# Kernel optimization log

Measured on AMD Instinct MI355X. Metric: run time of the kernel, lower is better.

The kernel has to match this reference:

```python
import jax, jax.numpy as jnp
import numpy as np

EMBED_DIM = 768
N_HEADS = 12
HEAD_DIM = EMBED_DIM // N_HEADS
SCALE = HEAD_DIM ** 0.5


def setup_inputs() -> dict:
    key = jax.random.key(0)
    k1, k2, k3 = jax.random.split(key, 3)
    x = jax.random.normal(k1, (2, 2048, EMBED_DIM), dtype=jnp.float32)
    # weights stored [in, out] so forward is x @ W (equivalent to torch Linear with W.T)
    w_qkv = jax.random.normal(k2, (EMBED_DIM, 3 * EMBED_DIM), dtype=jnp.float32) * (EMBED_DIM ** -0.5)
    w_proj = jax.random.normal(k3, (EMBED_DIM, EMBED_DIM), dtype=jnp.float32) * (EMBED_DIM ** -0.5)
    return {"x": x, "w_qkv": w_qkv, "w_proj": w_proj}


def reference(x, w_qkv, w_proj):
    B, N, C = x.shape
    qkv = x @ w_qkv  # [B, N, 3C]
    qkv = qkv.reshape(B, N, 3, N_HEADS, HEAD_DIM)
    qkv = jnp.transpose(qkv, (2, 0, 3, 1, 4))  # [3, B, H, N, hd]
    q, k, v = qkv[0], qkv[1], qkv[2]
    attn = jnp.einsum("bhnd,bhmd->bhnm", q, k) / SCALE  # [B, H, N, N]
    attn = jax.nn.softmax(attn, axis=-1)
    out = jnp.einsum("bhnm,bhmd->bhnd", attn, v)  # [B, H, N, hd]
    out = jnp.transpose(out, (0, 2, 1, 3)).reshape(B, N, C)
    return out @ w_proj
```

## Files before the change

kernel.cpp:

```cpp
#include <hip/hip_runtime.h>
#include <hip/hip_bf16.h>
#include <stdint.h>

typedef uint16_t u16;
typedef __attribute__((ext_vector_type(4))) float f32x4;
typedef __attribute__((ext_vector_type(8))) short bf16x8;

#define LOG2E 1.4426950408889634f

static __device__ __forceinline__ u16 f2b(float x){
  union { float f; uint32_t u; } a; a.f = x;
  uint32_t r = a.u + 0x7FFFu + ((a.u >> 16) & 1u);
  return (u16)(r >> 16);
}

static __device__ __forceinline__ uint32_t pkrhu(float lo, float hi){
  union { float f; uint32_t u; } a, b; a.f = lo; b.f = hi;
  return __builtin_amdgcn_perm(b.u + 0x8000u, a.u + 0x8000u, 0x07060302u);
}

#define GLD16(g, l) __builtin_amdgcn_global_load_lds((const __attribute__((address_space(1))) void*)(g), (__attribute__((address_space(3))) void*)(l), 16, 0, 0)

__global__ __launch_bounds__(256) void k_prep(const float* __restrict__ x, u16* __restrict__ Xb,
                                              const float* __restrict__ wqkv, u16* __restrict__ WqkvT,
                                              const float* __restrict__ wproj, u16* __restrict__ WprojT){
  __shared__ float t[32][33];
  const int bid = blockIdx.x, tid = threadIdx.x;
  if (bid < 1536){
    int i = bid * 256 + tid;
    const f32x4* p = (const f32x4*)(x + (size_t)i * 8);
    f32x4 a = p[0], b = p[1];
    u16 h[8];
#pragma unroll
    for (int j = 0; j < 4; ++j){ h[j] = f2b(a[j]); h[4+j] = f2b(b[j]); }
    *(bf16x8*)(Xb + (size_t)i * 8) = *(const bf16x8*)h;
    return;
  }
  const float* in; u16* out; int R, C, bx, by;
  if (bid < 1536 + 1728){
    int q = bid - 1536; in = wqkv; out = WqkvT; R = 768; C = 2304; bx = q % 72; by = q / 72;
  } else {
    int q = bid - 1536 - 1728; in = wproj; out = WprojT; R = 768; C = 768; bx = q % 24; by = q / 24;
  }
  int c0 = bx * 32, r0 = by * 32;
  int tx = tid & 31, ty = tid >> 5;
#pragma unroll
  for (int i = 0; i < 32; i += 8) t[ty + i][tx] = in[(size_t)(r0 + ty + i) * C + c0 + tx];
  __syncthreads();
#pragma unroll
  for (int i = 0; i < 32; i += 8) out[(size_t)(c0 + ty + i) * R + r0 + tx] = f2b(t[tx][ty + i]);
}

__global__ __launch_bounds__(256) void k_gemmqkv(const u16* __restrict__ A, const u16* __restrict__ Bt,
                                                 u16* __restrict__ Qp, u16* __restrict__ Kp, u16* __restrict__ Vtp){
  __shared__ __align__(16) u16 SM[14336];
  const int tid = threadIdx.x;
  const int w = tid >> 6, l = tid & 63;
  const int m0 = blockIdx.x * 128, n0 = blockIdx.y * 96;
  const int wm = (w >> 1) * 64, wn = (w & 1) * 48;
  const int lg = l >> 4, lr = l & 15;
  f32x4 acc[4][3] = {};

  const int tr = tid >> 2;
  const int soct = ((tid & 3) ^ (tr & 3)) * 8;
  const u16* a0 = A  + (size_t)(m0 + tr) * 768 + soct;
  const u16* a1 = A  + (size_t)(m0 + 64 + tr) * 768 + soct;
  const u16* b0 = Bt + (size_t)(n0 + tr) * 768 + soct;
  const u16* b1 = Bt + (size_t)(n0 + 64 + tr) * 768 + soct;
  u16* const A0d = SM + 0     + tid*8;  u16* const A0e = SM + 2048  + tid*8;
  u16* const A1d = SM + 4096  + tid*8;  u16* const A1e = SM + 6144  + tid*8;
  u16* const B0d = SM + 8192  + tid*8;  u16* const B0e = SM + 10240 + tid*8;
  u16* const B1d = SM + 11264 + tid*8;  u16* const B1e = SM + 13312 + tid*8;

#define QSTAGE0 do { GLD16(a0, A0d); GLD16(a1, A0e); GLD16(b0, B0d); if (tid < 128) GLD16(b1, B0e); \
                     a0 += 32; a1 += 32; b0 += 32; b1 += 32; } while(0)
#define QSTAGE1 do { GLD16(a0, A1d); GLD16(a1, A1e); GLD16(b0, B1d); if (tid < 128) GLD16(b1, B1e); \
                     a0 += 32; a1 += 32; b0 += 32; b1 += 32; } while(0)

  const int foct = (lg ^ (lr & 3)) * 8;

#define QCOMP(ABASE, BBASE) do {                                                            \
    bf16x8 af[4], bfr[3];                                                                   \
    _Pragma("unroll")                                                                       \
    for (int mf = 0; mf < 4; ++mf)                                                          \
      af[mf] = *(const bf16x8*)&SM[(ABASE) + (wm + mf*16 + lr) * 32 + foct];                \
    _Pragma("unroll")                                                                       \
    for (int nf = 0; nf < 3; ++nf)                                                          \
      bfr[nf] = *(const bf16x8*)&SM[(BBASE) + (wn + nf*16 + lr) * 32 + foct];               \
    _Pragma("unroll")                                                                       \
    for (int mf = 0; mf < 4; ++mf)                                                          \
      _Pragma("unroll")                                                                     \
      for (int nf = 0; nf < 3; ++nf)                                                        \
        acc[mf][nf] = __builtin_amdgcn_mfma_f32_16x16x32_bf16(af[mf], bfr[nf], acc[mf][nf], 0, 0, 0); \
  } while(0)

  QSTAGE0;
  __syncthreads();
  for (int i = 0; i < 12; ++i){
    QSTAGE1;
    QCOMP(0, 8192);
    __syncthreads();
    if (i < 11) QSTAGE0;
    QCOMP(4096, 11264);
    __syncthreads();
  }
#undef QSTAGE0
#undef QSTAGE1
#undef QCOMP

  const int which = n0 / 768;
  const int nl0 = n0 - which * 768;
  if (which < 2){
    u16* dst = (which == 0) ? Qp : Kp;
    const float sc = (which == 0) ? 0.125f * LOG2E : 1.0f;
#pragma unroll
    for (int mf = 0; mf < 4; ++mf)
#pragma unroll
      for (int nf = 0; nf < 3; ++nf)
#pragma unroll
        for (int r = 0; r < 4; ++r){
          int m = m0 + wm + mf*16 + lg*4 + r;
          int n = nl0 + wn + nf*16 + lr;
          int b = m >> 11, row = m & 2047, hh = n >> 6, d = n & 63;
          dst[(size_t)((b*12 + hh)*2048 + row) * 64 + d] = f2b(acc[mf][nf][r] * sc);
        }
  } else {
#pragma unroll
    for (int mf = 0; mf < 4; ++mf)
#pragma unroll
      for (int nf = 0; nf < 3; ++nf)
#pragma unroll
        for (int r = 0; r < 4; ++r){
          int mrow = wm + mf*16 + lg*4 + r;
          int c    = wn + nf*16 + lr;
          SM[c * 128 + mrow] = f2b(acc[mf][nf][r]);
        }
    __syncthreads();
#pragma unroll
    for (int rr = 0; rr < 6; ++rr){
      int c  = rr*16 + (tid >> 4);
      int mo = (tid & 15) * 8;
      bf16x8 v = *(const bf16x8*)&SM[c * 128 + mo];
      int n = nl0 + c, hh = n >> 6, d = n & 63;
      int m = m0 + mo, b = m >> 11, key = m & 2047;
      *(bf16x8*)&Vtp[(size_t)((b*12 + hh)*64 + d) * 2048 + key] = v;
    }
  }
}

__global__ __launch_bounds__(256) void k_gemm64(const u16* __restrict__ A, const u16* __restrict__ Bt,
                                                float* __restrict__ Co){
  __shared__ __align__(16) u16 SM[8192];
  u16* Al = SM; u16* Bl = SM + 4096;
  const int tid = threadIdx.x;
  const int w = tid >> 6, l = tid & 63;
  const int m0 = blockIdx.x * 64, n0 = blockIdx.y * 64;
  const int wm = (w >> 1) * 32, wn = (w & 1) * 32;
  const int lg = l >> 4, lr = l & 15;
  f32x4 acc[2][2] = {};
  const u16* asrc = A  + (size_t)(m0 + w*16 + (l >> 3)) * 768 + (l & 7) * 8;
  const u16* bsrc = Bt + (size_t)(n0 + w*16 + (l >> 3)) * 768 + (l & 7) * 8;
  for (int k0 = 0; k0 < 768; k0 += 64){
#pragma unroll
    for (int i = 0; i < 2; ++i){
      GLD16(asrc + (size_t)(i*8)*768 + k0, &Al[(w*16 + i*8) * 64]);
      GLD16(bsrc + (size_t)(i*8)*768 + k0, &Bl[(w*16 + i*8) * 64]);
    }
    __syncthreads();
    bf16x8 af[2][2], bfr[2][2];
#pragma unroll
    for (int mf = 0; mf < 2; ++mf)
#pragma unroll
      for (int ks = 0; ks < 2; ++ks){
        af[mf][ks]  = *(const bf16x8*)&Al[(wm + mf*16 + lr) * 64 + ks*32 + lg*8];
        bfr[mf][ks] = *(const bf16x8*)&Bl[(wn + mf*16 + lr) * 64 + ks*32 + lg*8];
      }
#pragma unroll
    for (int ks = 0; ks < 2; ++ks)
#pragma unroll
      for (int mf = 0; mf < 2; ++mf)
#pragma unroll
        for (int nf = 0; nf < 2; ++nf)
          acc[mf][nf] = __builtin_amdgcn_mfma_f32_16x16x32_bf16(af[mf][ks], bfr[nf][ks], acc[mf][nf], 0, 0, 0);
    __syncthreads();
  }
#pragma unroll
  for (int mf = 0; mf < 2; ++mf)
#pragma unroll
    for (int nf = 0; nf < 2; ++nf)
#pragma unroll
      for (int r = 0; r < 4; ++r)
        Co[(size_t)(m0 + wm + mf*16 + lg*4 + r) * 768 + n0 + wn + nf*16 + lr] = acc[mf][nf][r];
}

__global__ __launch_bounds__(512, 3) void k_attn(const u16* __restrict__ Qp, const u16* __restrict__ Kp,
                                                 const u16* __restrict__ Vtp, u16* __restrict__ AO){
  __shared__ __align__(16) u16 SM[24576];
  const int tid = threadIdx.x, w = tid >> 6, l = tid & 63;
  const int QH = w >> 1, KH = w & 1;
  const int lg = l >> 4, lr = l & 15;
  const int qt_b = blockIdx.x, bh = blockIdx.y;
  const int b = bh / 12, hh = bh - b * 12;
  const size_t base = (size_t)bh * (2048 * 64);
  const u16* Qg = Qp + base; const u16* Kg = Kp + base; const u16* Vg = Vtp + base;
  const int q0w = qt_b * 64 + QH * 16;
  const int rsw = (lr & 7) * 8;

  bf16x8 qf[2];
#pragma unroll
  for (int ks = 0; ks < 2; ++ks)
    qf[ks] = *(const bf16x8*)&Qg[(size_t)(q0w + lr) * 64 + ks*32 + lg*8];

  f32x4 oacc[4] = {};
  float lp = 0.f;

  const int p_  = tid >> 3;
  const int sk  = 32*(p_ >> 5) + 8*((p_ >> 2) & 3) + 4*((p_ >> 4) & 1) + (p_ & 3);
  const int cs8 = (((tid & 7) ^ (p_ & 7)) << 3);
  const u16* kp = Kg + (size_t)sk * 64 + cs8;
  const u16* vp = Vg + ((size_t)p_ << 11) + cs8;
  const int drow = p_ * 64;
  u16* const K0 = SM + 0     + drow;  u16* const V0 = SM + 12288 + drow;
  u16* const K1 = SM + 4096  + drow;  u16* const V1 = SM + 16384 + drow;
  u16* const K2 = SM + 8192  + drow;  u16* const V2 = SM + 20480 + drow;

  auto compute = [&](const u16* Kc, const u16* Vc){
    f32x4 s[2] = {};
    bf16x8 kfr[2][2];
#pragma unroll
    for (int kf = 0; kf < 2; ++kf)
#pragma unroll
      for (int ks = 0; ks < 2; ++ks)
        kfr[kf][ks] = *(const bf16x8*)&Kc[(KH*32 + kf*16 + lr) * 64 + ((ks*32 + lg*8) ^ rsw)];
    __builtin_amdgcn_s_setprio(1);
#pragma unroll
    for (int ks = 0; ks < 2; ++ks)
#pragma unroll
      for (int kf = 0; kf < 2; ++kf)
        s[kf] = __builtin_amdgcn_mfma_f32_16x16x32_bf16(kfr[kf][ks], qf[ks], s[kf], 0, 0, 0);
    __builtin_amdgcn_s_setprio(0);

    float p00 = __builtin_exp2f(s[0][0]);
    float p01 = __builtin_exp2f(s[0][1]);
    float p02 = __builtin_exp2f(s[0][2]);
    float p03 = __builtin_exp2f(s[0][3]);
    float p10 = __builtin_exp2f(s[1][0]);
    float p11 = __builtin_exp2f(s[1][1]);
    float p12 = __builtin_exp2f(s[1][2]);
    float p13 = __builtin_exp2f(s[1][3]);
    lp += ((p00 + p01) + (p02 + p03)) + ((p10 + p11) + (p12 + p13));
    union { uint32_t u[4]; bf16x8 v; } fr;
    fr.u[0] = pkrhu(p00, p01);
    fr.u[1] = pkrhu(p02, p03);
    fr.u[2] = pkrhu(p10, p11);
    fr.u[3] = pkrhu(p12, p13);

    bf16x8 vfr[4];
#pragma unroll
    for (int nf = 0; nf < 4; ++nf)
      vfr[nf] = *(const bf16x8*)&Vc[(nf*16 + lr) * 64 + ((KH*32 + lg*8) ^ rsw)];
    __builtin_amdgcn_s_setprio(1);
#pragma unroll
    for (int nf = 0; nf < 4; ++nf)
      oacc[nf] = __builtin_amdgcn_mfma_f32_16x16x32_bf16(vfr[nf], fr.v, oacc[nf], 0, 0, 0);
    __builtin_amdgcn_s_setprio(0);
  };

#define STAGE2(KD, VD) do { GLD16(kp, KD); GLD16(vp, VD); kp += 4096; vp += 64; } while(0)
#define BAR_CNT2  do { asm volatile("s_waitcnt vmcnt(2)" ::: "memory"); \
                       __builtin_amdgcn_s_barrier(); __builtin_amdgcn_sched_barrier(0); } while(0)
#define BAR_CNT0  do { asm volatile("s_waitcnt vmcnt(0)" ::: "memory"); \
                       __builtin_amdgcn_s_barrier(); __builtin_amdgcn_sched_barrier(0); } while(0)

  STAGE2(K0, V0);
  STAGE2(K1, V1);
  BAR_CNT2;

  for (int g = 0; g < 10; ++g){
    STAGE2(K2, V2);  compute(SM + 0,    SM + 12288);  BAR_CNT2;
    STAGE2(K0, V0);  compute(SM + 4096, SM + 16384);  BAR_CNT2;
    STAGE2(K1, V1);  compute(SM + 8192, SM + 20480);  BAR_CNT2;
  }
  compute(SM + 0,    SM + 12288);
  BAR_CNT0;
  compute(SM + 4096, SM + 16384);

#undef STAGE2
#undef BAR_CNT2
#undef BAR_CNT0

  float lt = lp;
  lt += __shfl_xor(lt, 16);
  lt += __shfl_xor(lt, 32);

  __syncthreads();
  float* Osc = (float*)SM;
  float* Lsc = Osc + 64 * 65;
  if (KH == 1){
#pragma unroll
    for (int nf = 0; nf < 4; ++nf)
#pragma unroll
      for (int r = 0; r < 4; ++r)
        Osc[(QH*16 + lr) * 65 + nf*16 + lg*4 + r] = oacc[nf][r];
    if (lg == 0) Lsc[QH*16 + lr] = lt;
  }
  __syncthreads();
  if (KH == 0){
    float inv = 1.0f / (lt + Lsc[QH*16 + lr]);
#pragma unroll
    for (int nf = 0; nf < 4; ++nf)
#pragma unroll
      for (int r = 0; r < 4; ++r){
        float o = oacc[nf][r] + Osc[(QH*16 + lr) * 65 + nf*16 + lg*4 + r];
        AO[(size_t)((b << 11) + q0w + lr) * 768 + hh*64 + nf*16 + lg*4 + r] = f2b(o * inv);
      }
  }
}

extern "C" void kernel_launch(void* const* d_in, const int* in_sizes, int n_in,
                              void* d_out, int out_size, void* d_ws, size_t ws_size,
                              hipStream_t stream){
  const float* x      = (const float*)d_in[0];
  const float* w_qkv  = (const float*)d_in[1];
  const float* w_proj = (const float*)d_in[2];
  float* out = (float*)d_out;
  char* ws = (char*)d_ws;
  u16* Xb     = (u16*)(ws + 0);
  u16* WqkvT  = (u16*)(ws + 6291456);
  u16* WprojT = (u16*)(ws + 9830400);
  u16* Qp     = (u16*)(ws + 11010048);
  u16* Kp     = (u16*)(ws + 17301504);
  u16* Vtp    = (u16*)(ws + 23592960);
  u16* AO     = (u16*)(ws + 29884416);

  k_prep<<<3840, 256, 0, stream>>>(x, Xb, w_qkv, WqkvT, w_proj, WprojT);
  k_gemmqkv<<<dim3(32, 24), 256, 0, stream>>>(Xb, WqkvT, Qp, Kp, Vtp);
  k_attn<<<dim3(32, 24), 512, 0, stream>>>(Qp, Kp, Vtp, AO);
  k_gemm64<<<dim3(64, 12), 256, 0, stream>>>(AO, WprojT, out);
}
```

Before: 87.34 us.

## Double-buffer output projection GEMM with swizzled LDS layout

Rewrites the 64x64 projection GEMM to use two LDS stages of K=32 each, issuing the next stage's global-to-LDS loads before computing on the current one. An XOR swizzle on the 16-byte octet index is meant to avoid LDS bank conflicts on the fragment reads. This overlaps memory latency with MFMA work, but the K step per barrier shrinks, so the loop runs more barriers.

Result: faster. 85.03 us (-2.6%).

```diff
diff --git a/kernel.cpp b/kernel.cpp
--- a/kernel.cpp
+++ b/kernel.cpp
@@ -151,39 +151,56 @@
 __global__ __launch_bounds__(256) void k_gemm64(const u16* __restrict__ A, const u16* __restrict__ Bt,
                                                 float* __restrict__ Co){
   __shared__ __align__(16) u16 SM[8192];
-  u16* Al = SM; u16* Bl = SM + 4096;
   const int tid = threadIdx.x;
   const int w = tid >> 6, l = tid & 63;
   const int m0 = blockIdx.x * 64, n0 = blockIdx.y * 64;
   const int wm = (w >> 1) * 32, wn = (w & 1) * 32;
   const int lg = l >> 4, lr = l & 15;
   f32x4 acc[2][2] = {};
-  const u16* asrc = A  + (size_t)(m0 + w*16 + (l >> 3)) * 768 + (l & 7) * 8;
-  const u16* bsrc = Bt + (size_t)(n0 + w*16 + (l >> 3)) * 768 + (l & 7) * 8;
-  for (int k0 = 0; k0 < 768; k0 += 64){
-#pragma unroll
-    for (int i = 0; i < 2; ++i){
-      GLD16(asrc + (size_t)(i*8)*768 + k0, &Al[(w*16 + i*8) * 64]);
-      GLD16(bsrc + (size_t)(i*8)*768 + k0, &Bl[(w*16 + i*8) * 64]);
-    }
-    __syncthreads();
-    bf16x8 af[2][2], bfr[2][2];
-#pragma unroll
-    for (int mf = 0; mf < 2; ++mf)
-#pragma unroll
-      for (int ks = 0; ks < 2; ++ks){
-        af[mf][ks]  = *(const bf16x8*)&Al[(wm + mf*16 + lr) * 64 + ks*32 + lg*8];
-        bfr[mf][ks] = *(const bf16x8*)&Bl[(wn + mf*16 + lr) * 64 + ks*32 + lg*8];
-      }
-#pragma unroll
-    for (int ks = 0; ks < 2; ++ks)
-#pragma unroll
-      for (int mf = 0; mf < 2; ++mf)
-#pragma unroll
-        for (int nf = 0; nf < 2; ++nf)
-          acc[mf][nf] = __builtin_amdgcn_mfma_f32_16x16x32_bf16(af[mf][ks], bfr[nf][ks], acc[mf][nf], 0, 0, 0);
-    __syncthreads();
-  }
+
+  const int tr = tid >> 2;
+  const int soct = ((tid & 3) ^ (tr & 3)) * 8;
+  const u16* a0 = A  + (size_t)(m0 + tr) * 768 + soct;
+  const u16* b0 = Bt + (size_t)(n0 + tr) * 768 + soct;
+  u16* const A0d = SM + 0    + tid*8;
+  u16* const A1d = SM + 2048 + tid*8;
+  u16* const B0d = SM + 4096 + tid*8;
+  u16* const B1d = SM + 6144 + tid*8;
+
+#define PSTAGE0 do { GLD16(a0, A0d); GLD16(b0, B0d); a0 += 32; b0 += 32; } while(0)
+#define PSTAGE1 do { GLD16(a0, A1d); GLD16(b0, B1d); a0 += 32; b0 += 32; } while(0)
+
+  const int foct = (lg ^ (lr & 3)) * 8;
+
+#define PCOMP(ABASE, BBASE) do {                                                            \
+    bf16x8 af[2], bfr[2];                                                                   \
+    _Pragma("unroll")                                                                       \
+    for (int mf = 0; mf < 2; ++mf)                                                          \
+      af[mf] = *(const bf16x8*)&SM[(ABASE) + (wm + mf*16 + lr) * 32 + foct];                \
+    _Pragma("unroll")                                                                       \
+    for (int nf = 0; nf < 2; ++nf)                                                          \
+      bfr[nf] = *(const bf16x8*)&SM[(BBASE) + (wn + nf*16 + lr) * 32 + foct];               \
+    _Pragma("unroll")                                                                       \
+    for (int mf = 0; mf < 2; ++mf)                                                          \
+      _Pragma("unroll")                                                                     \
+      for (int nf = 0; nf < 2; ++nf)                                                        \
+        acc[mf][nf] = __builtin_amdgcn_mfma_f32_16x16x32_bf16(af[mf], bfr[nf], acc[mf][nf], 0, 0, 0); \
+  } while(0)
+
+  PSTAGE0;
+  __syncthreads();
+  for (int i = 0; i < 12; ++i){
+    PSTAGE1;
+    PCOMP(0, 4096);
+    __syncthreads();
+    if (i < 11) PSTAGE0;
+    PCOMP(2048, 6144);
+    __syncthreads();
+  }
+#undef PSTAGE0
+#undef PSTAGE1
+#undef PCOMP
+
 #pragma unroll
   for (int mf = 0; mf < 2; ++mf)
 #pragma unroll
```
